# Kernel tuning notes

Measured on AMD Instinct MI355X. Metric: run time of the kernel, lower is better.

The kernel has to match this reference:

```python
import jax, jax.numpy as jnp
import numpy as np
import math

D = 256; NH = 8; NG = 64; META = 6

def _linear(x, w, b):
    return x @ w.T + b

def setup_inputs():
    key = jax.random.key(0)
    ks = jax.random.split(key, 12)
    B, T, TG = 32, 4096, 1024
    def rn(k, shape, s=0.02):
        return jax.random.normal(k, shape, dtype=jnp.float32) * s
    q = jax.random.normal(ks[0], (1, NG, D), dtype=jnp.float32)
    q = q / jnp.clip(jnp.linalg.norm(q, axis=-1, keepdims=True), 1e-6)
    # fibonacci unit sphere anchor, scaled by 0.4
    idx = jnp.arange(NG, dtype=jnp.float32)
    golden = (1.0 + math.sqrt(5.0)) / 2.0
    theta = 2.0 * math.pi * idx / golden
    z = jnp.clip(1.0 - (2.0 * idx + 1.0) / NG, -1.0 + 1e-6, 1.0 - 1e-6)
    r = jnp.sqrt(jnp.clip(1.0 - z * z, 0.0))
    pts = jnp.stack([r * jnp.cos(theta), r * jnp.sin(theta), z], axis=-1)
    pts = pts / jnp.clip(jnp.linalg.norm(pts, axis=-1, keepdims=True), 1e-6)
    p0 = (pts * 0.4)[None]
    ph_b2 = jnp.array([0.0] * 6 + [-2.0] * 4, dtype=jnp.float32)
    return dict(
        local_feat=jax.random.normal(ks[1], (B, D, T), dtype=jnp.float32),
        global_feat=jax.random.normal(ks[2], (B, D, TG), dtype=jnp.float32),
        meta=jax.random.uniform(ks[3], (B, META), dtype=jnp.float32),
        queries=q, p0_anchor=p0,
        in_proj_w=rn(ks[4], (3 * D, D)), in_proj_b=jnp.zeros((3 * D,), jnp.float32),
        out_proj_w=rn(ks[5], (D, D)), out_proj_b=jnp.zeros((D,), jnp.float32),
        ln_g=jnp.ones((D,), jnp.float32), ln_b=jnp.zeros((D,), jnp.float32),
        meta_w=rn(ks[6], (D, META)), meta_b=jnp.zeros((D,), jnp.float32),
        temporal_w=rn(ks[7], (D, D)), temporal_b=jnp.zeros((D,), jnp.float32),
        shift_w=rn(ks[8], (3, D)), shift_b=jnp.zeros((3,), jnp.float32),
        ph_w1=rn(ks[9], (D // 2, D)), ph_b1=jnp.zeros((D // 2,), jnp.float32),
        ph_w2=rn(ks[10], (10, D // 2)), ph_b2=ph_b2,
        wave_delay_scale=jnp.float32(0.1),
        envelope_bias=jnp.float32(0.5),
    )

def reference(local_feat, global_feat, meta, queries, p0_anchor, in_proj_w, in_proj_b,
              out_proj_w, out_proj_b, ln_g, ln_b, meta_w, meta_b, temporal_w, temporal_b,
              shift_w, shift_b, ph_w1, ph_b1, ph_w2, ph_b2, wave_delay_scale, envelope_bias):
    B, _, T = local_feat.shape
    DH = D // NH
    kv = jnp.transpose(global_feat, (0, 2, 1))                        # [B,TG,D]
    q = jnp.broadcast_to(queries, (B, NG, D))
    wq, wk, wv = in_proj_w[:D], in_proj_w[D:2 * D], in_proj_w[2 * D:]
    bq, bk, bv = in_proj_b[:D], in_proj_b[D:2 * D], in_proj_b[2 * D:]
    qh = _linear(q, wq, bq).reshape(B, NG, NH, DH)
    kh = _linear(kv, wk, bk).reshape(B, -1, NH, DH)
    vh = _linear(kv, wv, bv).reshape(B, -1, NH, DH)
    attn = jax.nn.softmax(jnp.einsum('bqhd,bkhd->bhqk', qh, kh) / math.sqrt(DH), axis=-1)
    ctx = jnp.einsum('bhqk,bkhd->bqhd', attn, vh).reshape(B, NG, D)
    x = q + _linear(ctx, out_proj_w, out_proj_b)
    mu = x.mean(-1, keepdims=True)
    var = ((x - mu) ** 2).mean(-1, keepdims=True)
    q_static = (x - mu) / jnp.sqrt(var + 1e-5) * ln_g + ln_b
    q_static = q_static + jax.nn.gelu(_linear(meta, meta_w, meta_b), approximate=False)[:, None, :]
    params = _linear(jax.nn.gelu(_linear(q_static, ph_w1, ph_b1), approximate=False), ph_w2, ph_b2)
    p0_delta = jnp.tanh(params[..., 0:3]) * 0.2
    heart_shift = jnp.tanh(_linear(global_feat.mean(-1), shift_w, shift_b)) * 0.3
    p_pos = p0_anchor + p0_delta + heart_shift[:, None, :]            # [B,NG,3]
    dnorm = jnp.clip(jnp.linalg.norm(params[..., 3:6], axis=-1, keepdims=True), 1e-6)
    dipole_dir = params[..., 3:6] / dnorm
    volume_xyz = jax.nn.sigmoid(params[..., 6:9]) * 0.5 + 0.001
    amplitude = jax.nn.sigmoid(params[..., 9]) + 1e-4                 # [B,NG]
    tw = _linear(q_static, temporal_w, temporal_b)                    # [B,NG,D]
    temporal_logits = jnp.einsum('bnc,bct->bnt', tw, local_feat) / math.sqrt(D)
    idx_sa = jnp.argmax(amplitude, axis=1)                            # [B]
    p_sa = jnp.take_along_axis(p_pos, idx_sa[:, None, None], axis=1)  # [B,1,3]
    dist = jnp.linalg.norm(p_pos - p_sa, axis=-1)                     # [B,NG]
    delay = jnp.clip(jax.nn.softplus(wave_delay_scale) * dist, 0.0, 0.1)
    base_x = jnp.linspace(-1.0, 1.0, T)
    grid_x = base_x[None, None, :] - delay[..., None]                 # [B,NG,T]
    # grid_sample(bilinear, zeros, align_corners=True): grid_y hits rows exactly,
    # so it reduces to 1D linear interp along time with zero padding.
    x_pix = (grid_x + 1.0) * 0.5 * (T - 1)
    x0 = jnp.floor(x_pix).astype(jnp.int32)
    x1 = x0 + 1
    w1 = x_pix - x0.astype(x_pix.dtype)
    w0 = 1.0 - w1
    def samp(xi):
        g = jnp.take_along_axis(temporal_logits, jnp.clip(xi, 0, T - 1), axis=-1)
        return g * ((xi >= 0) & (xi <= T - 1)).astype(g.dtype)
    shifted = w0 * samp(x0) + w1 * samp(x1)
    envelope_t = jax.nn.sigmoid(shifted + envelope_bias)              # [B,NG,T]
    return amplitude, p_pos, dipole_dir, volume_xyz, envelope_t
```

## Files before the change

kernel.cpp:

```cpp
#include <hip/hip_runtime.h>
#include <hip/hip_bf16.h>
#include <math.h>

typedef __hip_bfloat16 bf16;
typedef short s16x8 __attribute__((ext_vector_type(8)));
typedef float f32x4 __attribute__((ext_vector_type(4)));

#define NDIM 256
#define NTG 1024
#define NT 4096

__device__ __forceinline__ float gelu_exact(float x) {
    return 0.5f * x * (1.0f + erff(x * 0.70710678118654752440f));
}
__device__ __forceinline__ float sigmoidf_(float x) {
    return 1.0f / (1.0f + __expf(-x));
}
__device__ __forceinline__ short f2bf_s(float x) {
    union { bf16 h; short s; } cv;
    cv.h = __float2bfloat16(x);
    return cv.s;
}
__device__ __forceinline__ float bf2f(short s) {
    union { bf16 h; short s; } cv;
    cv.s = s;
    return __bfloat162float(cv.h);
}

__global__ __launch_bounds__(256) void k_prep(
        const float* __restrict__ ipw, const float* __restrict__ opw,
        const float* __restrict__ twm, const float* __restrict__ pw1,
        const float* __restrict__ queries, const float* __restrict__ ipb,
        float* __restrict__ opwT, float* __restrict__ twT, float* __restrict__ pw1T,
        bf16* __restrict__ wkvK, bf16* __restrict__ wkvV,
        float* __restrict__ qh) {
    __shared__ float qrow[256];
    int blk = blockIdx.x, tid = threadIdx.x;
    if (blk < 384) {
        int id = blk * 256 + tid;
        if (id < 65536) {
            int k = id >> 8, c = id & 255;
            opwT[id] = opw[c * 256 + k];
            twT[id]  = twm[c * 256 + k];
        } else {
            int id2 = id - 65536;
            int k = id2 >> 7, m = id2 & 127;
            pw1T[id2] = pw1[m * 256 + k];
        }
    } else if (blk < 640) {
        int id = (blk - 384) * 256 + tid;
        wkvK[id] = __float2bfloat16(ipw[65536 + id]);
        wkvV[id] = __float2bfloat16(ipw[131072 + id]);
    } else {
        int n = blk - 640, c = tid;
        qrow[c] = queries[n * 256 + c];
        __syncthreads();
        float s = ipb[c];
        const float* wr = ipw + c * 256;
        for (int k = 0; k < 256; ++k) s += qrow[k] * wr[k];
        qh[n * 256 + c] = s;
    }
}

__global__ __launch_bounds__(256) void k_kv(
        const float* __restrict__ gf, const short* __restrict__ wkvK,
        const short* __restrict__ wkvV, const float* __restrict__ ipb,
        short* __restrict__ kvh, short* __restrict__ vTg,
        float* __restrict__ partial) {
    __shared__ __align__(16) short gfs[64 * 264];
    int blk = blockIdx.x, tid = threadIdx.x;
    int b = blk >> 4, tt = blk & 15;
    int t0 = tt * 64;
    int f4 = tid & 15, grp = tid >> 4;
    #pragma unroll 4
    for (int p = 0; p < 16; ++p) {
        int row = p * 16 + grp;
        float4 v = *(const float4*)&gf[((size_t)(b * 256 + row)) * 1024 + t0 + f4 * 4];
        gfs[(f4 * 4 + 0) * 264 + row] = f2bf_s(v.x);
        gfs[(f4 * 4 + 1) * 264 + row] = f2bf_s(v.y);
        gfs[(f4 * 4 + 2) * 264 + row] = f2bf_s(v.z);
        gfs[(f4 * 4 + 3) * 264 + row] = f2bf_s(v.w);
        float ps = v.x + v.y + v.z + v.w;
        ps += __shfl_xor(ps, 1); ps += __shfl_xor(ps, 2);
        ps += __shfl_xor(ps, 4); ps += __shfl_xor(ps, 8);
        if (f4 == 0) partial[(b * 256 + row) * 16 + tt] = ps;
    }
    __syncthreads();
    int w = tid >> 6, lane = tid & 63, lm = lane & 15, quad = lane >> 4;
    int n0 = w * 64;
    f32x4 acc[4][4];
    #pragma unroll
    for (int ni = 0; ni < 4; ++ni)
        #pragma unroll
        for (int mt = 0; mt < 4; ++mt) acc[ni][mt] = (f32x4)(0.0f);
    #pragma unroll
    for (int ks = 0; ks < 8; ++ks) {
        int c = ks * 32 + quad * 8;
        s16x8 gm[4];
        #pragma unroll
        for (int mt = 0; mt < 4; ++mt)
            gm[mt] = *(const s16x8*)&gfs[(mt * 16 + lm) * 264 + c];
        #pragma unroll
        for (int ni = 0; ni < 4; ++ni) {
            s16x8 aw = *(const s16x8*)&wkvK[(n0 + ni * 16 + lm) * 256 + c];
            #pragma unroll
            for (int mt = 0; mt < 4; ++mt)
                acc[ni][mt] = __builtin_amdgcn_mfma_f32_16x16x32_bf16(aw, gm[mt], acc[ni][mt], 0, 0, 0);
        }
    }
    #pragma unroll
    for (int ni = 0; ni < 4; ++ni) {
        int nb4 = n0 + ni * 16 + quad * 4;
        float4 bias = *(const float4*)&ipb[256 + nb4];
        #pragma unroll
        for (int mt = 0; mt < 4; ++mt) {
            int t = t0 + mt * 16 + lm;
            ushort4 o;
            o.x = (unsigned short)f2bf_s(acc[ni][mt][0] + bias.x);
            o.y = (unsigned short)f2bf_s(acc[ni][mt][1] + bias.y);
            o.z = (unsigned short)f2bf_s(acc[ni][mt][2] + bias.z);
            o.w = (unsigned short)f2bf_s(acc[ni][mt][3] + bias.w);
            *(ushort4*)&kvh[((size_t)(b * 1024 + t)) * 256 + nb4] = o;
        }
    }
    #pragma unroll
    for (int mt = 0; mt < 4; ++mt)
        #pragma unroll
        for (int ni = 0; ni < 4; ++ni) acc[mt][ni] = (f32x4)(0.0f);
    #pragma unroll
    for (int ks = 0; ks < 8; ++ks) {
        int c = ks * 32 + quad * 8;
        s16x8 gm[4];
        #pragma unroll
        for (int mt = 0; mt < 4; ++mt)
            gm[mt] = *(const s16x8*)&gfs[(mt * 16 + lm) * 264 + c];
        #pragma unroll
        for (int ni = 0; ni < 4; ++ni) {
            s16x8 bw = *(const s16x8*)&wkvV[(n0 + ni * 16 + lm) * 256 + c];
            #pragma unroll
            for (int mt = 0; mt < 4; ++mt)
                acc[mt][ni] = __builtin_amdgcn_mfma_f32_16x16x32_bf16(gm[mt], bw, acc[mt][ni], 0, 0, 0);
        }
    }
    #pragma unroll
    for (int ni = 0; ni < 4; ++ni) {
        int nv = n0 + ni * 16 + lm;
        float bias = ipb[512 + nv];
        #pragma unroll
        for (int mt = 0; mt < 4; ++mt) {
            int t4 = t0 + mt * 16 + quad * 4;
            ushort4 o;
            o.x = (unsigned short)f2bf_s(acc[mt][ni][0] + bias);
            o.y = (unsigned short)f2bf_s(acc[mt][ni][1] + bias);
            o.z = (unsigned short)f2bf_s(acc[mt][ni][2] + bias);
            o.w = (unsigned short)f2bf_s(acc[mt][ni][3] + bias);
            *(ushort4*)&vTg[((size_t)(b * 256 + nv)) * 1024 + t4] = o;
        }
    }
}

__global__ __launch_bounds__(256) void k_attn(
        const short* __restrict__ kvh, const short* __restrict__ vTg,
        const float* __restrict__ qh,
        const float* __restrict__ meta, const float* __restrict__ mw,
        const float* __restrict__ mb, const float* __restrict__ partial,
        const float* __restrict__ sw, const float* __restrict__ sb,
        float* __restrict__ o_half, float* __restrict__ l_half,
        float* __restrict__ metag, float* __restrict__ hshift) {
    __shared__ short pT[4][64 * 40];
    __shared__ float obuf[4][64 * 36];
    __shared__ float lbuf[4 * 64];
    if (blockIdx.z >= 32) {
        int b = (blockIdx.z - 32) * 16 + blockIdx.y * 2 + blockIdx.x;
        int c = threadIdx.x;
        float m = 0.f;
        const float* pp = partial + (b * 256 + c) * 16;
        #pragma unroll
        for (int t = 0; t < 16; ++t) m += pp[t];
        lbuf[c] = m * (1.0f / 1024.0f);
        float s = mb[c];
        #pragma unroll
        for (int j = 0; j < 6; ++j) s += meta[b * 6 + j] * mw[c * 6 + j];
        metag[b * 256 + c] = gelu_exact(s);
        __syncthreads();
        if (c < 3) {
            float t = sb[c];
            for (int k = 0; k < 256; ++k) t += lbuf[k] * sw[c * 256 + k];
            hshift[b * 4 + c] = tanhf(t) * 0.3f;
        }
        return;
    }
    int tid = threadIdx.x;
    int w = tid >> 6, lane = tid & 63, lm = lane & 15, quad = lane >> 4;
    int half = blockIdx.x, h = blockIdx.y, b = blockIdx.z;
    s16x8 aq[4];
    #pragma unroll
    for (int mt = 0; mt < 4; ++mt) {
        const float4* qp = (const float4*)(qh + (mt * 16 + lm) * 256 + h * 32 + quad * 8);
        float4 qa = qp[0], qb = qp[1];
        aq[mt][0] = f2bf_s(qa.x); aq[mt][1] = f2bf_s(qa.y);
        aq[mt][2] = f2bf_s(qa.z); aq[mt][3] = f2bf_s(qa.w);
        aq[mt][4] = f2bf_s(qb.x); aq[mt][5] = f2bf_s(qb.y);
        aq[mt][6] = f2bf_s(qb.z); aq[mt][7] = f2bf_s(qb.w);
    }
    f32x4 acco[2][4];
    #pragma unroll
    for (int dt = 0; dt < 2; ++dt)
        #pragma unroll
        for (int qt = 0; qt < 4; ++qt) acco[dt][qt] = (f32x4)(0.0f);
    float lp[4][4];
    #pragma unroll
    for (int mt = 0; mt < 4; ++mt)
        #pragma unroll
        for (int r = 0; r < 4; ++r) lp[mt][r] = 0.f;
    const float scale = 0.17677669529663687f;
    int kb = half * 512 + w * 128;
    for (int ch = 0; ch < 4; ++ch) {
        int n0 = kb + ch * 32;
        #pragma unroll
        for (int nt = 0; nt < 2; ++nt) {
            int key = n0 + nt * 16 + lm;
            s16x8 bk = *(const s16x8*)&kvh[((size_t)(b * 1024 + key)) * 256 + h * 32 + quad * 8];
            f32x4 zero = {0.f, 0.f, 0.f, 0.f};
            #pragma unroll
            for (int mt = 0; mt < 4; ++mt) {
                f32x4 S = __builtin_amdgcn_mfma_f32_16x16x32_bf16(aq[mt], bk, zero, 0, 0, 0);
                #pragma unroll
                for (int r = 0; r < 4; ++r) {
                    float e = __expf(S[r] * scale);
                    lp[mt][r] += e;
                    pT[w][(mt * 16 + quad * 4 + r) * 40 + nt * 16 + lm] = f2bf_s(e);
                }
            }
        }
        s16x8 av[2], bp[4];
        #pragma unroll
        for (int dt = 0; dt < 2; ++dt)
            av[dt] = *(const s16x8*)&vTg[((size_t)(b * 256 + h * 32 + dt * 16 + lm)) * 1024 + n0 + quad * 8];
        #pragma unroll
        for (int qt = 0; qt < 4; ++qt)
            bp[qt] = *(const s16x8*)&pT[w][(qt * 16 + lm) * 40 + quad * 8];
        #pragma unroll
        for (int dt = 0; dt < 2; ++dt)
            #pragma unroll
            for (int qt = 0; qt < 4; ++qt)
                acco[dt][qt] = __builtin_amdgcn_mfma_f32_16x16x32_bf16(av[dt], bp[qt], acco[dt][qt], 0, 0, 0);
    }
    #pragma unroll
    for (int mt = 0; mt < 4; ++mt)
        #pragma unroll
        for (int r = 0; r < 4; ++r) {
            float v = lp[mt][r];
            v += __shfl_xor(v, 1); v += __shfl_xor(v, 2);
            v += __shfl_xor(v, 4); v += __shfl_xor(v, 8);
            lp[mt][r] = v;
        }
    #pragma unroll
    for (int dt = 0; dt < 2; ++dt)
        #pragma unroll
        for (int qt = 0; qt < 4; ++qt) {
            int q = qt * 16 + lm;
            float4 t;
            t.x = acco[dt][qt][0]; t.y = acco[dt][qt][1];
            t.z = acco[dt][qt][2]; t.w = acco[dt][qt][3];
            *(float4*)&obuf[w][q * 36 + dt * 16 + quad * 4] = t;
        }
    if (lm == 0) {
        #pragma unroll
        for (int mt = 0; mt < 4; ++mt)
            #pragma unroll
            for (int r = 0; r < 4; ++r)
                lbuf[w * 64 + mt * 16 + quad * 4 + r] = lp[mt][r];
    }
    __syncthreads();
    int q = tid & 63, dg = tid >> 6;
    int blk = (b * 8 + h) * 2 + half;
    float l = lbuf[q] + lbuf[64 + q] + lbuf[128 + q] + lbuf[192 + q];
    float o[8];
    #pragma unroll
    for (int j = 0; j < 8; ++j) o[j] = 0.f;
    #pragma unroll
    for (int w2 = 0; w2 < 4; ++w2) {
        const float* src = &obuf[w2][q * 36 + dg * 8];
        #pragma unroll
        for (int j = 0; j < 8; ++j) o[j] += src[j];
    }
    float* dst = &o_half[(((size_t)blk * 64) + q) * 32 + dg * 8];
    #pragma unroll
    for (int j = 0; j < 8; ++j) dst[j] = o[j];
    if (dg == 0) l_half[blk * 64 + q] = l;
}

__global__ __launch_bounds__(256) void k_post(
        const float* __restrict__ o_half, const float* __restrict__ l_half,
        const float* __restrict__ queries,
        const float* __restrict__ opwT, const float* __restrict__ opb,
        const float* __restrict__ lng, const float* __restrict__ lnb,
        const float* __restrict__ metag, const float* __restrict__ hshift,
        const float* __restrict__ twT, const float* __restrict__ tbv,
        const float* __restrict__ pw1T, const float* __restrict__ pb1,
        const float* __restrict__ pw2, const float* __restrict__ pb2,
        const float* __restrict__ p0a,
        bf16* __restrict__ twbf, float* __restrict__ out_amp,
        float* __restrict__ out_ppos, float* __restrict__ out_dip,
        float* __restrict__ out_vol) {
    __shared__ float cs[4][256];
    __shared__ float xs[4][256];
    __shared__ float qs[4][256];
    __shared__ float h1[4][128];
    __shared__ float ps[4][10];
    int tid = threadIdx.x;
    int n0 = blockIdx.x * 4, b = blockIdx.y;
    {
        int h = tid >> 5, d = tid & 31;
        int blk0 = (b * 8 + h) * 2;
        #pragma unroll
        for (int r = 0; r < 4; ++r) {
            int q = n0 + r;
            float l = l_half[blk0 * 64 + q] + l_half[(blk0 + 1) * 64 + q];
            float v0 = o_half[(((size_t)blk0 * 64) + q) * 32 + d];
            float v1 = o_half[(((size_t)(blk0 + 1) * 64) + q) * 32 + d];
            cs[r][tid] = (v0 + v1) / l;
        }
    }
    __syncthreads();
    {
        int c = tid;
        float a[4];
        #pragma unroll
        for (int nn = 0; nn < 4; ++nn) a[nn] = opb[c];
        for (int k = 0; k < 256; ++k) {
            float w = opwT[k * 256 + c];
            #pragma unroll
            for (int nn = 0; nn < 4; ++nn) a[nn] += cs[nn][k] * w;
        }
        #pragma unroll
        for (int nn = 0; nn < 4; ++nn)
            xs[nn][c] = queries[(n0 + nn) * 256 + c] + a[nn];
    }
    __syncthreads();
    {
        int w = tid >> 6, lane = tid & 63;
        int nr = w;
        float x0 = xs[nr][lane], x1 = xs[nr][lane + 64],
              x2 = xs[nr][lane + 128], x3 = xs[nr][lane + 192];
        float s = x0 + x1 + x2 + x3;
        #pragma unroll
        for (int off = 32; off >= 1; off >>= 1) s += __shfl_xor(s, off);
        float mu = s * (1.0f / 256.0f);
        float e0 = x0 - mu, e1 = x1 - mu, e2 = x2 - mu, e3 = x3 - mu;
        float v = e0*e0 + e1*e1 + e2*e2 + e3*e3;
        #pragma unroll
        for (int off = 32; off >= 1; off >>= 1) v += __shfl_xor(v, off);
        float rstd = 1.0f / sqrtf(v * (1.0f / 256.0f) + 1e-5f);
        #pragma unroll
        for (int j = 0; j < 4; ++j) {
            int c = lane + 64 * j;
            qs[nr][c] = (xs[nr][c] - mu) * rstd * lng[c] + lnb[c] + metag[b * 256 + c];
        }
    }
    __syncthreads();
    {
        int c = tid;
        float a[4];
        #pragma unroll
        for (int nn = 0; nn < 4; ++nn) a[nn] = tbv[c];
        for (int k = 0; k < 256; ++k) {
            float w = twT[k * 256 + c];
            #pragma unroll
            for (int nn = 0; nn < 4; ++nn) a[nn] += qs[nn][k] * w;
        }
        #pragma unroll
        for (int nn = 0; nn < 4; ++nn)
            twbf[(size_t)(b * 64 + n0 + nn) * 256 + c] = __float2bfloat16(a[nn]);
    }
    {
        int m = tid & 127, g = tid >> 7;
        float a[2];
        #pragma unroll
        for (int q2 = 0; q2 < 2; ++q2) a[q2] = pb1[m];
        for (int k = 0; k < 256; ++k) {
            float w = pw1T[k * 128 + m];
            #pragma unroll
            for (int q2 = 0; q2 < 2; ++q2) a[q2] += qs[g * 2 + q2][k] * w;
        }
        #pragma unroll
        for (int q2 = 0; q2 < 2; ++q2) h1[g * 2 + q2][m] = gelu_exact(a[q2]);
    }
    __syncthreads();
    if (tid < 40) {
        int nr = tid / 10, j = tid % 10;
        float s = pb2[j];
        for (int m = 0; m < 128; ++m) s += h1[nr][m] * pw2[j * 128 + m];
        ps[nr][j] = s;
    }
    __syncthreads();
    if (tid < 4) {
        int nr = tid;
        int gn = b * 64 + n0 + nr;
        #pragma unroll
        for (int j = 0; j < 3; ++j) {
            float delta = tanhf(ps[nr][j]) * 0.2f;
            out_ppos[gn * 3 + j] = p0a[(n0 + nr) * 3 + j] + delta + hshift[b * 4 + j];
        }
        float d0 = ps[nr][3], d1 = ps[nr][4], d2 = ps[nr][5];
        float dn = fmaxf(sqrtf(d0 * d0 + d1 * d1 + d2 * d2), 1e-6f);
        out_dip[gn * 3 + 0] = d0 / dn;
        out_dip[gn * 3 + 1] = d1 / dn;
        out_dip[gn * 3 + 2] = d2 / dn;
        #pragma unroll
        for (int j = 0; j < 3; ++j)
            out_vol[gn * 3 + j] = sigmoidf_(ps[nr][6 + j]) * 0.5f + 0.001f;
        out_amp[gn] = sigmoidf_(ps[nr][9]) + 0.0001f;
    }
}

__global__ __launch_bounds__(256) void k_temporal(
        const float* __restrict__ lf, const short* __restrict__ twbf,
        short* __restrict__ logits) {
    __shared__ __align__(16) short tws[64 * 264];
    __shared__ __align__(16) short lfs[2][32 * 132];
    int tid = threadIdx.x;
    int t0 = blockIdx.x * 128, b = blockIdx.y;
    int wave = tid >> 6, lane = tid & 63;
    int lm = lane & 15, quad = lane >> 4;

    #pragma unroll
    for (int i = 0; i < 8; ++i) {
        int id = i * 256 + tid;
        int n = id >> 5, c8 = id & 31;
        s16x8 v = *(const s16x8*)&twbf[(size_t)(b * 64 + n) * 256 + c8 * 8];
        *(s16x8*)&tws[n * 264 + c8 * 8] = v;
    }

    float4 fr[4];
    #pragma unroll
    for (int r = 0; r < 4; ++r) {
        int id = r * 256 + tid;
        int c = id >> 5, t4 = id & 31;
        fr[r] = *(const float4*)&lf[((size_t)(b * 256 + c)) * 4096 + t0 + t4 * 4];
    }
    #pragma unroll
    for (int r = 0; r < 4; ++r) {
        int id = r * 256 + tid;
        int c = id >> 5, t4 = id & 31;
        ushort4 o;
        o.x = (unsigned short)f2bf_s(fr[r].x);
        o.y = (unsigned short)f2bf_s(fr[r].y);
        o.z = (unsigned short)f2bf_s(fr[r].z);
        o.w = (unsigned short)f2bf_s(fr[r].w);
        *(ushort4*)&lfs[0][c * 132 + t4 * 4] = o;
    }

    f32x4 acc[2][4];
    #pragma unroll
    for (int mi = 0; mi < 2; ++mi)
        #pragma unroll
        for (int ni = 0; ni < 4; ++ni) acc[mi][ni] = (f32x4)(0.0f);

    __syncthreads();

    for (int ksi = 0; ksi < 8; ++ksi) {
        int cur = ksi & 1;
        if (ksi < 7) {
            int c0n = (ksi + 1) * 32;
            #pragma unroll
            for (int r = 0; r < 4; ++r) {
                int id = r * 256 + tid;
                int c = id >> 5, t4 = id & 31;
                fr[r] = *(const float4*)&lf[((size_t)(b * 256 + c0n + c)) * 4096 + t0 + t4 * 4];
            }
        }
        int c0 = ksi * 32;
        #pragma unroll
        for (int mi = 0; mi < 2; ++mi) {
            int tl = wave * 32 + mi * 16 + lm;
            s16x8 af;
            #pragma unroll
            for (int j = 0; j < 8; ++j)
                af[j] = lfs[cur][(quad * 8 + j) * 132 + tl];
            #pragma unroll
            for (int ni = 0; ni < 4; ++ni) {
                s16x8 bfr = *(const s16x8*)&tws[(ni * 16 + lm) * 264 + c0 + quad * 8];
                acc[mi][ni] = __builtin_amdgcn_mfma_f32_16x16x32_bf16(af, bfr, acc[mi][ni], 0, 0, 0);
            }
        }
        if (ksi < 7) {
            #pragma unroll
            for (int r = 0; r < 4; ++r) {
                int id = r * 256 + tid;
                int c = id >> 5, t4 = id & 31;
                ushort4 o;
                o.x = (unsigned short)f2bf_s(fr[r].x);
                o.y = (unsigned short)f2bf_s(fr[r].y);
                o.z = (unsigned short)f2bf_s(fr[r].z);
                o.w = (unsigned short)f2bf_s(fr[r].w);
                *(ushort4*)&lfs[cur ^ 1][c * 132 + t4 * 4] = o;
            }
        }
        __syncthreads();
    }
    #pragma unroll
    for (int mi = 0; mi < 2; ++mi) {
        #pragma unroll
        for (int ni = 0; ni < 4; ++ni) {
            int n = ni * 16 + lm;
            int t = t0 + wave * 32 + mi * 16 + quad * 4;
            ushort4 o;
            o.x = (unsigned short)f2bf_s(acc[mi][ni][0] * 0.0625f);
            o.y = (unsigned short)f2bf_s(acc[mi][ni][1] * 0.0625f);
            o.z = (unsigned short)f2bf_s(acc[mi][ni][2] * 0.0625f);
            o.w = (unsigned short)f2bf_s(acc[mi][ni][3] * 0.0625f);
            *(ushort4*)&logits[(size_t)(b * 64 + n) * 4096 + t] = o;
        }
    }
}

__global__ __launch_bounds__(256) void k_envelope(
        const short* __restrict__ logits,
        const float* __restrict__ out_amp,
        const float* __restrict__ out_ppos,
        const float* __restrict__ wds,
        const float* __restrict__ ebp,
        float* __restrict__ env) {
    __shared__ __align__(16) short ls[208 + 4096 + 16];
    int bn = blockIdx.x;
    int b = bn >> 6, n = bn & 63;
    int tid = threadIdx.x;
    int lane = tid & 63;
    if (tid < 208) ls[tid] = 0;
    if (tid < 16) ls[208 + 4096 + tid] = 0;
    const short* gl = logits + (size_t)bn * 4096;
    {
        s16x8 v0 = *(const s16x8*)&gl[tid * 16];
        s16x8 v1 = *(const s16x8*)&gl[tid * 16 + 8];
        *(s16x8*)&ls[208 + tid * 16] = v0;
        *(s16x8*)&ls[208 + tid * 16 + 8] = v1;
    }
    float v = out_amp[b * 64 + lane];
    int idx = lane;
    #pragma unroll
    for (int off = 1; off < 64; off <<= 1) {
        float ov = __shfl_xor(v, off);
        int oi = __shfl_xor(idx, off);
        if (ov > v || (ov == v && oi < idx)) { v = ov; idx = oi; }
    }
    float dx = out_ppos[(b * 64 + n) * 3 + 0] - out_ppos[(b * 64 + idx) * 3 + 0];
    float dy = out_ppos[(b * 64 + n) * 3 + 1] - out_ppos[(b * 64 + idx) * 3 + 1];
    float dz = out_ppos[(b * 64 + n) * 3 + 2] - out_ppos[(b * 64 + idx) * 3 + 2];
    float dist = sqrtf(dx * dx + dy * dy + dz * dz);
    float sp = log1pf(expf(wds[0]));
    float dl = fminf(fmaxf(sp * dist, 0.f), 0.1f);
    float eb = ebp[0];
    __syncthreads();
    #pragma unroll
    for (int g = 0; g < 4; ++g) {
        int t_base = g * 1024 + tid * 4;
        float ov4[4];
        #pragma unroll
        for (int u = 0; u < 4; ++u) {
            int t = t_base + u;
            float xb = fmaf((float)t, 2.0f / 4095.0f, -1.0f);
            float xp = (xb - dl + 1.0f) * 2047.5f;
            float x0f = floorf(xp);
            int x0 = (int)x0f;
            float w1 = xp - x0f, w0 = 1.0f - w1;
            float g0 = bf2f(ls[208 + x0]);
            float g1 = bf2f(ls[208 + x0 + 1]);
            float sh = w0 * g0 + w1 * g1;
            ov4[u] = 1.0f / (1.0f + __expf(-(sh + eb)));
        }
        float4 o; o.x = ov4[0]; o.y = ov4[1]; o.z = ov4[2]; o.w = ov4[3];
        *reinterpret_cast<float4*>(&env[(size_t)bn * 4096 + t_base]) = o;
    }
}

extern "C" void kernel_launch(void* const* d_in, const int* in_sizes, int n_in,
                              void* d_out, int out_size, void* d_ws, size_t ws_size,
                              hipStream_t stream) {
    const float* lf   = (const float*)d_in[0];
    const float* gf   = (const float*)d_in[1];
    const float* meta = (const float*)d_in[2];
    const float* qrs  = (const float*)d_in[3];
    const float* p0a  = (const float*)d_in[4];
    const float* ipw  = (const float*)d_in[5];
    const float* ipb  = (const float*)d_in[6];
    const float* opw  = (const float*)d_in[7];
    const float* opb  = (const float*)d_in[8];
    const float* lng  = (const float*)d_in[9];
    const float* lnb  = (const float*)d_in[10];
    const float* mw   = (const float*)d_in[11];
    const float* mb   = (const float*)d_in[12];
    const float* twm  = (const float*)d_in[13];
    const float* tbv  = (const float*)d_in[14];
    const float* sw   = (const float*)d_in[15];
    const float* sb   = (const float*)d_in[16];
    const float* pw1  = (const float*)d_in[17];
    const float* pb1  = (const float*)d_in[18];
    const float* pw2  = (const float*)d_in[19];
    const float* pb2  = (const float*)d_in[20];
    const float* wds  = (const float*)d_in[21];
    const float* ebp  = (const float*)d_in[22];

    char* ws = (char*)d_ws;
    short* kvh    = (short*)(ws);
    short* vTg    = (short*)(ws + 16777216);
    short* logits = (short*)(ws + 50331648);
    float* o_half = (float*)(ws + 67108864);
    float* l_half = (float*)(ws + 71303168);
    short* twbf   = (short*)(ws + 71434240);
    float* qh     = (float*)(ws + 72482816);
    float* metag  = (float*)(ws + 72581120);
    float* hshift = (float*)(ws + 72613888);
    float* opwT   = (float*)(ws + 72614400);
    float* twT    = (float*)(ws + 72876544);
    float* pw1T   = (float*)(ws + 73138688);
    short* wkvK   = (short*)(ws + 73269760);
    short* wkvV   = (short*)(ws + 73400832);
    float* partial= (float*)(ws + 73531904);

    float* out_amp  = (float*)d_out;
    float* out_ppos = out_amp + 2048;
    float* out_dip  = out_amp + 8192;
    float* out_vol  = out_amp + 14336;
    float* env      = out_amp + 20480;

    k_prep<<<704, 256, 0, stream>>>(ipw, opw, twm, pw1, qrs, ipb,
                                    opwT, twT, pw1T, (bf16*)wkvK, (bf16*)wkvV, qh);
    k_kv<<<512, 256, 0, stream>>>(gf, wkvK, wkvV, ipb, kvh, vTg, partial);
    k_attn<<<dim3(2, 8, 34), 256, 0, stream>>>(kvh, vTg, qh, meta, mw, mb, partial,
                                               sw, sb, o_half, l_half, metag, hshift);
    k_post<<<dim3(16, 32), 256, 0, stream>>>(o_half, l_half, qrs, opwT, opb, lng, lnb,
                                             metag, hshift, twT, tbv, pw1T, pb1, pw2, pb2,
                                             p0a, (bf16*)twbf, out_amp, out_ppos,
                                             out_dip, out_vol);
    k_temporal<<<dim3(32, 32), 256, 0, stream>>>(lf, twbf, logits);
    k_envelope<<<2048, 256, 0, stream>>>(logits, out_amp, out_ppos, wds, ebp, env);
}
```

Baseline: 371.6 us.

## Move weight transposes into k_kv and double queries per k_post block

```diff
diff --git a/kernel.cpp b/kernel.cpp
--- a/kernel.cpp
+++ b/kernel.cpp
@@ -28,47 +28,49 @@
 }
 
 __global__ __launch_bounds__(256) void k_prep(
-        const float* __restrict__ ipw, const float* __restrict__ opw,
-        const float* __restrict__ twm, const float* __restrict__ pw1,
-        const float* __restrict__ queries, const float* __restrict__ ipb,
-        float* __restrict__ opwT, float* __restrict__ twT, float* __restrict__ pw1T,
-        bf16* __restrict__ wkvK, bf16* __restrict__ wkvV,
-        float* __restrict__ qh) {
-    __shared__ float qrow[256];
-    int blk = blockIdx.x, tid = threadIdx.x;
-    if (blk < 384) {
-        int id = blk * 256 + tid;
-        if (id < 65536) {
-            int k = id >> 8, c = id & 255;
-            opwT[id] = opw[c * 256 + k];
-            twT[id]  = twm[c * 256 + k];
-        } else {
-            int id2 = id - 65536;
-            int k = id2 >> 7, m = id2 & 127;
-            pw1T[id2] = pw1[m * 256 + k];
-        }
-    } else if (blk < 640) {
-        int id = (blk - 384) * 256 + tid;
-        wkvK[id] = __float2bfloat16(ipw[65536 + id]);
-        wkvV[id] = __float2bfloat16(ipw[131072 + id]);
-    } else {
-        int n = blk - 640, c = tid;
-        qrow[c] = queries[n * 256 + c];
-        __syncthreads();
-        float s = ipb[c];
-        const float* wr = ipw + c * 256;
-        for (int k = 0; k < 256; ++k) s += qrow[k] * wr[k];
-        qh[n * 256 + c] = s;
-    }
+        const float* __restrict__ ipw,
+        bf16* __restrict__ wkvK, bf16* __restrict__ wkvV) {
+    int id = blockIdx.x * 256 + threadIdx.x;
+    wkvK[id] = __float2bfloat16(ipw[65536 + id]);
+    wkvV[id] = __float2bfloat16(ipw[131072 + id]);
 }
 
 __global__ __launch_bounds__(256) void k_kv(
         const float* __restrict__ gf, const short* __restrict__ wkvK,
         const short* __restrict__ wkvV, const float* __restrict__ ipb,
+        const float* __restrict__ ipw, const float* __restrict__ opw,
+        const float* __restrict__ twm, const float* __restrict__ pw1,
+        const float* __restrict__ queries,
         short* __restrict__ kvh, short* __restrict__ vTg,
-        float* __restrict__ partial) {
+        float* __restrict__ partial,
+        float* __restrict__ opwT, float* __restrict__ twT,
+        float* __restrict__ pw1T, float* __restrict__ qh) {
     __shared__ __align__(16) short gfs[64 * 264];
     int blk = blockIdx.x, tid = threadIdx.x;
+    if (blk >= 512) {
+        if (blk < 896) {
+            int id = (blk - 512) * 256 + tid;
+            if (id < 65536) {
+                int k = id >> 8, cc = id & 255;
+                opwT[id] = opw[cc * 256 + k];
+                twT[id]  = twm[cc * 256 + k];
+            } else {
+                int id2 = id - 65536;
+                int k = id2 >> 7, m = id2 & 127;
+                pw1T[id2] = pw1[m * 256 + k];
+            }
+        } else {
+            float* qrow = (float*)gfs;
+            int n = blk - 896, cc = tid;
+            qrow[cc] = queries[n * 256 + cc];
+            __syncthreads();
+            float s = ipb[cc];
+            const float* wr = ipw + cc * 256;
+            for (int k = 0; k < 256; ++k) s += qrow[k] * wr[k];
+            qh[n * 256 + cc] = s;
+        }
+        return;
+    }
     int b = blk >> 4, tt = blk & 15;
     int t0 = tt * 64;
     int f4 = tid & 15, grp = tid >> 4;
@@ -291,7 +293,7 @@
     if (dg == 0) l_half[blk * 64 + q] = l;
 }
 
-__global__ __launch_bounds__(256) void k_post(
+__global__ __launch_bounds__(512) void k_post(
         const float* __restrict__ o_half, const float* __restrict__ l_half,
         const float* __restrict__ queries,
         const float* __restrict__ opwT, const float* __restrict__ opb,
@@ -304,46 +306,56 @@
         bf16* __restrict__ twbf, float* __restrict__ out_amp,
         float* __restrict__ out_ppos, float* __restrict__ out_dip,
         float* __restrict__ out_vol) {
-    __shared__ float cs[4][256];
-    __shared__ float xs[4][256];
-    __shared__ float qs[4][256];
-    __shared__ float h1[4][128];
-    __shared__ float ps[4][10];
+    __shared__ float cs[8][256];
+    __shared__ float xs[8][256];
+    __shared__ float qs[8][256];
+    __shared__ float pbuf[2][8][256];
+    __shared__ float h1[8][128];
+    __shared__ float ps[8][10];
     int tid = threadIdx.x;
-    int n0 = blockIdx.x * 4, b = blockIdx.y;
-    {
-        int h = tid >> 5, d = tid & 31;
+    int n0 = blockIdx.x * 8, b = blockIdx.y;
+    int rr = tid >> 8, c = tid & 255;
+    {
+        int h = c >> 5, d = c & 31;
         int blk0 = (b * 8 + h) * 2;
         #pragma unroll
-        for (int r = 0; r < 4; ++r) {
+        for (int i = 0; i < 4; ++i) {
+            int r = rr * 4 + i;
             int q = n0 + r;
             float l = l_half[blk0 * 64 + q] + l_half[(blk0 + 1) * 64 + q];
             float v0 = o_half[(((size_t)blk0 * 64) + q) * 32 + d];
             float v1 = o_half[(((size_t)(blk0 + 1) * 64) + q) * 32 + d];
-            cs[r][tid] = (v0 + v1) / l;
-        }
-    }
-    __syncthreads();
-    {
-        int c = tid;
-        float a[4];
-        #pragma unroll
-        for (int nn = 0; nn < 4; ++nn) a[nn] = opb[c];
-        for (int k = 0; k < 256; ++k) {
+            cs[r][c] = (v0 + v1) / l;
+        }
+    }
+    __syncthreads();
+    {
+        float a[8];
+        #pragma unroll
+        for (int nn = 0; nn < 8; ++nn) a[nn] = 0.f;
+        int k0 = rr * 128;
+        for (int k = k0; k < k0 + 128; ++k) {
             float w = opwT[k * 256 + c];
             #pragma unroll
-            for (int nn = 0; nn < 4; ++nn) a[nn] += cs[nn][k] * w;
-        }
-        #pragma unroll
-        for (int nn = 0; nn < 4; ++nn)
-            xs[nn][c] = queries[(n0 + nn) * 256 + c] + a[nn];
+            for (int nn = 0; nn < 8; ++nn) a[nn] += cs[nn][k] * w;
+        }
+        #pragma unroll
+        for (int nn = 0; nn < 8; ++nn) pbuf[rr][nn][c] = a[nn];
+    }
+    __syncthreads();
+    {
+        #pragma unroll
+        for (int i = 0; i < 4; ++i) {
+            int nn = rr * 4 + i;
+            xs[nn][c] = queries[(n0 + nn) * 256 + c] + opb[c]
+                      + pbuf[0][nn][c] + pbuf[1][nn][c];
+        }
     }
     __syncthreads();
     {
         int w = tid >> 6, lane = tid & 63;
-        int nr = w;
-        float x0 = xs[nr][lane], x1 = xs[nr][lane + 64],
-              x2 = xs[nr][lane + 128], x3 = xs[nr][lane + 192];
+        float x0 = xs[w][lane], x1 = xs[w][lane + 64],
+              x2 = xs[w][lane + 128], x3 = xs[w][lane + 192];
         float s = x0 + x1 + x2 + x3;
         #pragma unroll
         for (int off = 32; off >= 1; off >>= 1) s += __shfl_xor(s, off);
@@ -355,47 +367,66 @@
         float rstd = 1.0f / sqrtf(v * (1.0f / 256.0f) + 1e-5f);
         #pragma unroll
         for (int j = 0; j < 4; ++j) {
-            int c = lane + 64 * j;
-            qs[nr][c] = (xs[nr][c] - mu) * rstd * lng[c] + lnb[c] + metag[b * 256 + c];
-        }
-    }
-    __syncthreads();
-    {
-        int c = tid;
+            int cc = lane + 64 * j;
+            qs[w][cc] = (xs[w][cc] - mu) * rstd * lng[cc] + lnb[cc] + metag[b * 256 + cc];
+        }
+    }
+    __syncthreads();
+    {
+        float a[8];
+        #pragma unroll
+        for (int nn = 0; nn < 8; ++nn) a[nn] = 0.f;
+        int k0 = rr * 128;
+        for (int k = k0; k < k0 + 128; ++k) {
+            float w = twT[k * 256 + c];
+            #pragma unroll
+            for (int nn = 0; nn < 8; ++nn) a[nn] += qs[nn][k] * w;
+        }
+        #pragma unroll
+        for (int nn = 0; nn < 8; ++nn) pbuf[rr][nn][c] = a[nn];
+    }
+    __syncthreads();
+    {
+        #pragma unroll
+        for (int i = 0; i < 4; ++i) {
+            int nn = rr * 4 + i;
+            twbf[(size_t)(b * 64 + n0 + nn) * 256 + c] =
+                __float2bfloat16(tbv[c] + pbuf[0][nn][c] + pbuf[1][nn][c]);
+        }
+    }
+    __syncthreads();
+    {
+        int m = tid & 127, qq = (tid >> 7) & 1;
         float a[4];
         #pragma unroll
-        for (int nn = 0; nn < 4; ++nn) a[nn] = tbv[c];
-        for (int k = 0; k < 256; ++k) {
-            float w = twT[k * 256 + c];
-            #pragma unroll
-            for (int nn = 0; nn < 4; ++nn) a[nn] += qs[nn][k] * w;
-        }
-        #pragma unroll
-        for (int nn = 0; nn < 4; ++nn)
-            twbf[(size_t)(b * 64 + n0 + nn) * 256 + c] = __float2bfloat16(a[nn]);
-    }
-    {
-        int m = tid & 127, g = tid >> 7;
-        float a[2];
-        #pragma unroll
-        for (int q2 = 0; q2 < 2; ++q2) a[q2] = pb1[m];
-        for (int k = 0; k < 256; ++k) {
+        for (int i = 0; i < 4; ++i) a[i] = 0.f;
+        int k0 = rr * 128;
+        for (int k = k0; k < k0 + 128; ++k) {
             float w = pw1T[k * 128 + m];
             #pragma unroll
-            for (int q2 = 0; q2 < 2; ++q2) a[q2] += qs[g * 2 + q2][k] * w;
-        }
-        #pragma unroll
-        for (int q2 = 0; q2 < 2; ++q2) h1[g * 2 + q2][m] = gelu_exact(a[q2]);
-    }
-    __syncthreads();
-    if (tid < 40) {
+            for (int i = 0; i < 4; ++i) a[i] += qs[qq * 4 + i][k] * w;
+        }
+        #pragma unroll
+        for (int i = 0; i < 4; ++i) pbuf[rr][qq * 4 + i][m] = a[i];
+    }
+    __syncthreads();
+    {
+        #pragma unroll
+        for (int u = 0; u < 2; ++u) {
+            int id = u * 512 + tid;
+            int nr = id >> 7, m = id & 127;
+            h1[nr][m] = gelu_exact(pb1[m] + pbuf[0][nr][m] + pbuf[1][nr][m]);
+        }
+    }
+    __syncthreads();
+    if (tid < 80) {
         int nr = tid / 10, j = tid % 10;
         float s = pb2[j];
         for (int m = 0; m < 128; ++m) s += h1[nr][m] * pw2[j * 128 + m];
         ps[nr][j] = s;
     }
     __syncthreads();
-    if (tid < 4) {
+    if (tid < 8) {
         int nr = tid;
         int gn = b * 64 + n0 + nr;
         #pragma unroll
@@ -625,15 +656,15 @@
     float* out_vol  = out_amp + 14336;
     float* env      = out_amp + 20480;
 
-    k_prep<<<704, 256, 0, stream>>>(ipw, opw, twm, pw1, qrs, ipb,
-                                    opwT, twT, pw1T, (bf16*)wkvK, (bf16*)wkvV, qh);
-    k_kv<<<512, 256, 0, stream>>>(gf, wkvK, wkvV, ipb, kvh, vTg, partial);
+    k_prep<<<256, 256, 0, stream>>>(ipw, (bf16*)wkvK, (bf16*)wkvV);
+    k_kv<<<960, 256, 0, stream>>>(gf, wkvK, wkvV, ipb, ipw, opw, twm, pw1, qrs,
+                                  kvh, vTg, partial, opwT, twT, pw1T, qh);
     k_attn<<<dim3(2, 8, 34), 256, 0, stream>>>(kvh, vTg, qh, meta, mw, mb, partial,
                                                sw, sb, o_half, l_half, metag, hshift);
-    k_post<<<dim3(16, 32), 256, 0, stream>>>(o_half, l_half, qrs, opwT, opb, lng, lnb,
-                                             metag, hshift, twT, tbv, pw1T, pb1, pw2, pb2,
-                                             p0a, (bf16*)twbf, out_amp, out_ppos,
-                                             out_dip, out_vol);
+    k_post<<<dim3(8, 32), 512, 0, stream>>>(o_half, l_half, qrs, opwT, opb, lng, lnb,
+                                            metag, hshift, twT, tbv, pw1T, pb1, pw2, pb2,
+                                            p0a, (bf16*)twbf, out_amp, out_ppos,
+                                            out_dip, out_vol);
     k_temporal<<<dim3(32, 32), 256, 0, stream>>>(lf, twbf, logits);
     k_envelope<<<2048, 256, 0, stream>>>(logits, out_amp, out_ppos, wds, ebp, env);
 }
```

Result: faster. 359.3 us (-3.3%).
